# Kernel optimization log

Measured on AMD Instinct MI355X. Metric: run time of the kernel, lower is better.

## Reference

```python
import jax, jax.numpy as jnp
import numpy as np

N = 30000      # nodes
E = 480000     # edges (before self-loops)
G = 30         # graphs
DIN = 256      # input_dim
DH = 64        # hidden_dim (per-head out channels)
H = 8          # heads in layers 0,1; last layer has 1 head


def _glorot(key, shape):
    fan_in, fan_out = shape[0], shape[-1]
    s = jnp.sqrt(2.0 / (fan_in + fan_out))
    return jax.random.normal(key, shape, dtype=jnp.float32) * s


def setup_inputs() -> dict:
    key = jax.random.key(0)
    ks = jax.random.split(key, 32)
    inp = {
        'x': jax.random.normal(ks[0], (N, DIN), dtype=jnp.float32),
        'edge_index': jax.random.randint(ks[1], (2, E), 0, N, dtype=jnp.int64),
        'batch': jnp.sort(jax.random.randint(ks[2], (N,), 0, G, dtype=jnp.int64)),
        # GAT layer 0: in=256 -> 8 heads x 64
        'W0': _glorot(ks[3], (DIN, H * DH)),
        'as0': _glorot(ks[4], (H, DH)), 'ad0': _glorot(ks[5], (H, DH)),
        'b0': jnp.zeros((H * DH,), jnp.float32),
        # GAT layer 1: in=512 -> 8 heads x 64
        'W1': _glorot(ks[6], (H * DH, H * DH)),
        'as1': _glorot(ks[7], (H, DH)), 'ad1': _glorot(ks[8], (H, DH)),
        'b1': jnp.zeros((H * DH,), jnp.float32),
        # GAT layer 2: in=512 -> 1 head x 64
        'W2': _glorot(ks[9], (H * DH, DH)),
        'as2': _glorot(ks[10], (1, DH)), 'ad2': _glorot(ks[11], (1, DH)),
        'b2': jnp.zeros((DH,), jnp.float32),
        # batch norms (feature sizes match actual activations)
        'bn0_g': jnp.ones((H * DH,), jnp.float32), 'bn0_b': jnp.zeros((H * DH,), jnp.float32),
        'bn1_g': jnp.ones((H * DH,), jnp.float32), 'bn1_b': jnp.zeros((H * DH,), jnp.float32),
        'bn2_g': jnp.ones((DH,), jnp.float32), 'bn2_b': jnp.zeros((DH,), jnp.float32),
        'ln_g': jnp.ones((DH,), jnp.float32), 'ln_b': jnp.zeros((DH,), jnp.float32),
        'fc1_w': _glorot(ks[12], (DH, DH // 2)), 'fc1_b': jnp.zeros((DH // 2,), jnp.float32),
        'fc2_w': _glorot(ks[13], (DH // 2, 2)), 'fc2_b': jnp.zeros((2,), jnp.float32),
    }
    return inp


def _gat(x, src, dst, W, a_src, a_dst, bias, heads):
    # x: [N, Fin]; project to [N, heads, DH]
    h = (x @ W).reshape(N, heads, DH)
    s_src = jnp.sum(h * a_src, axis=-1)  # [N, heads]
    s_dst = jnp.sum(h * a_dst, axis=-1)  # [N, heads]
    e = jax.nn.leaky_relu(s_src[src] + s_dst[dst], 0.2)  # [Etot, heads]
    # segment softmax over edges grouped by destination node
    m = jax.ops.segment_max(e, dst, num_segments=N)
    p = jnp.exp(e - m[dst])
    denom = jax.ops.segment_sum(p, dst, num_segments=N)
    alpha = p / (denom[dst] + 1e-16)
    out = jax.ops.segment_sum(h[src] * alpha[:, :, None], dst, num_segments=N)
    return out.reshape(N, heads * DH) + bias


def _bn(x, g, b):
    m = jnp.mean(x, axis=0)
    v = jnp.var(x, axis=0)
    return (x - m) / jnp.sqrt(v + 1e-5) * g + b


def _forward(x, edge_index, batch,
             W0, as0, ad0, b0, W1, as1, ad1, b1, W2, as2, ad2, b2,
             bn0_g, bn0_b, bn1_g, bn1_b, bn2_g, bn2_b,
             ln_g, ln_b, fc1_w, fc1_b, fc2_w, fc2_b):
    loops = jnp.arange(N, dtype=edge_index.dtype)
    src = jnp.concatenate([edge_index[0], loops])
    dst = jnp.concatenate([edge_index[1], loops])
    # layer 0: 256 -> 512; no residual (dim mismatch)
    x1 = jax.nn.elu(_bn(_gat(x, src, dst, W0, as0, ad0, b0, H), bn0_g, bn0_b))
    # layer 1: 512 -> 512; residual
    x2 = jax.nn.elu(_bn(_gat(x1, src, dst, W1, as1, ad1, b1, H), bn1_g, bn1_b)) + x1
    # layer 2 (single head): 512 -> 64; no residual
    x3 = jax.nn.elu(_bn(_gat(x2, src, dst, W2, as2, ad2, b2, 1), bn2_g, bn2_b))
    # layer norm
    mu = jnp.mean(x3, axis=-1, keepdims=True)
    var = jnp.var(x3, axis=-1, keepdims=True)
    xl = (x3 - mu) / jnp.sqrt(var + 1e-5) * ln_g + ln_b
    # global mean pool over graphs
    sums = jax.ops.segment_sum(xl, batch, num_segments=G)
    cnt = jax.ops.segment_sum(jnp.ones((N, 1), xl.dtype), batch, num_segments=G)
    pooled = sums / jnp.maximum(cnt, 1.0)
    hdd = jax.nn.elu(pooled @ fc1_w + fc1_b)
    logits = hdd @ fc2_w + fc2_b
    return jax.nn.log_softmax(logits, axis=1)


def reference(x, edge_index, batch,
              W0, as0, ad0, b0, W1, as1, ad1, b1, W2, as2, ad2, b2,
              bn0_g, bn0_b, bn1_g, bn1_b, bn2_g, bn2_b,
              ln_g, ln_b, fc1_w, fc1_b, fc2_w, fc2_b):
    return _forward(x, edge_index, batch,
                    W0, as0, ad0, b0, W1, as1, ad1, b1, W2, as2, ad2, b2,
                    bn0_g, bn0_b, bn1_g, bn1_b, bn2_g, bn2_b,
                    ln_g, ln_b, fc1_w, fc1_b, fc2_w, fc2_b)
```

## Files before the change

### kernel.cpp

```cpp
#include <hip/hip_runtime.h>
#include <math.h>

#define NODES 30000
#define NEDGE 480000
#define ETOT  (NODES + NEDGE)
#define NGRAPH 30
#define DIN 256
#define DH 64
#define CAP 128

typedef __bf16 bf16x8 __attribute__((ext_vector_type(8)));
typedef float  f32x4  __attribute__((ext_vector_type(4)));

static __device__ __forceinline__ float elu_f(float x){ return x > 0.f ? x : expm1f(x); }
static __device__ __forceinline__ float bf_lo(unsigned v){ return __uint_as_float(v << 16); }
static __device__ __forceinline__ float bf_hi(unsigned v){ return __uint_as_float(v & 0xffff0000u); }
static __device__ __forceinline__ unsigned pack_bf2(float a, float b){
  __bf16 ob[2] = {(__bf16)a, (__bf16)b};
  return *(unsigned*)ob;
}
static __device__ __forceinline__ void load_lds16(const __bf16* g, __bf16* l){
  __builtin_amdgcn_global_load_lds(
      (const __attribute__((address_space(1))) void*)g,
      (__attribute__((address_space(3))) void*)l, 16, 0, 0);
}

__global__ void k_scan(const int* __restrict__ deg, int* __restrict__ rowptr){
  __shared__ int s[1024];
  int t = threadIdx.x;
  const int CH = (NODES + 1023) / 1024;
  int base = t * CH;
  int local = 0;
  for (int i = 0; i < CH; i++){ int idx = base + i; if (idx < NODES) local += deg[idx]; }
  s[t] = local; __syncthreads();
  for (int off = 1; off < 1024; off <<= 1){
    int v = (t >= off) ? s[t - off] : 0;
    __syncthreads();
    s[t] += v;
    __syncthreads();
  }
  int run = s[t] - local;
  for (int i = 0; i < CH; i++){
    int idx = base + i;
    if (idx < NODES){ rowptr[idx] = run; run += deg[idx]; }
  }
  if (t == 1023) rowptr[NODES] = s[1023];
}

__global__ void k_fill(const int* __restrict__ ei, const int* __restrict__ rowptr,
                       int* __restrict__ cursor, int* __restrict__ colA){
  int e = blockIdx.x*256 + threadIdx.x;
  if (e >= ETOT) return;
  int src, dst;
  if (e < NEDGE){ src = ei[e]; dst = ei[NEDGE + e]; }
  else          { src = e - NEDGE; dst = src; }
  int pos = atomicAdd(&cursor[dst], 1);
  colA[rowptr[dst] + pos] = src;
}

#define NCAST4 (NODES*DIN/4)
#define TW0 (512*256)
#define TW1 (512*512)
#define TW2 (64*512)
#define PREPW (NCAST4 + TW0 + TW1 + TW2)
__global__ void k_prep(const float* __restrict__ x, __bf16* __restrict__ xb0,
                       const float* __restrict__ W0, const float* __restrict__ W1,
                       const float* __restrict__ W2, __bf16* __restrict__ Wt0,
                       __bf16* __restrict__ Wt1, __bf16* __restrict__ Wt2,
                       const int* __restrict__ ei, int* __restrict__ deg){
  int idx = blockIdx.x*256 + threadIdx.x;
  if (idx < NCAST4){
    float4 v = ((const float4*)x)[idx];
    __bf16 o[4] = {(__bf16)v.x, (__bf16)v.y, (__bf16)v.z, (__bf16)v.w};
    *(uint2*)(xb0 + (size_t)idx*4) = *(const uint2*)o;
    return;
  }
  int j = idx - NCAST4;
  if (j < TW0){
    int n = j >> 8, k = j & 255;
    Wt0[j] = (__bf16)W0[(size_t)k*512 + n];
    return;
  }
  j -= TW0;
  if (j < TW1){
    int n = j >> 9, k = j & 511;
    Wt1[j] = (__bf16)W1[(size_t)k*512 + n];
    return;
  }
  j -= TW1;
  if (j < TW2){
    int n = j >> 9, k = j & 511;
    Wt2[j] = (__bf16)W2[(size_t)k*64 + n];
    return;
  }
  j -= TW2;
  if (j < ETOT){
    int dst = (j < NEDGE) ? ei[NEDGE + j] : (j - NEDGE);
    atomicAdd(&deg[dst], 1);
  }
}

__global__ __launch_bounds__(256) void k_gemm_bf16(const __bf16* __restrict__ A,
    const __bf16* __restrict__ Bt, __bf16* __restrict__ C,
    const float* __restrict__ asrc, const float* __restrict__ adst,
    float* __restrict__ ssrc, float* __restrict__ sdst, int heads,
    int M, int N, int K){
  __shared__ __align__(16) __bf16 As[128*64];
  __shared__ __align__(16) __bf16 Bs[128*64];
  int tid  = threadIdx.x;
  int lane = tid & 63, wave = tid >> 6;
  int wr = wave >> 1, wc = wave & 1;
  int q = lane >> 4, r = lane & 15;
  int rowBase = blockIdx.y * 128, colBase = blockIdx.x * 128;
  f32x4 acc[4][4] = {};
  for (int k0 = 0; k0 < K; k0 += 64){
    #pragma unroll
    for (int p = 0; p < 4; p++){
      int lin = p*256 + tid;
      int rr = lin >> 3, ko = (lin & 7) * 8;
      int gr = rowBase + rr; if (gr >= M) gr = M - 1;
      load_lds16(A + (size_t)gr*K + k0 + ko, As + lin*8);
      int gn = colBase + rr; if (gn >= N) gn = N - 1;
      load_lds16(Bt + (size_t)gn*K + k0 + ko, Bs + lin*8);
    }
    __syncthreads();
    #pragma unroll
    for (int kk = 0; kk < 2; kk++){
      bf16x8 af[4], bfr[4];
      #pragma unroll
      for (int i = 0; i < 4; i++) af[i]  = *(const bf16x8*)(&As[(wr*64 + i*16 + r)*64 + kk*32 + q*8]);
      #pragma unroll
      for (int j = 0; j < 4; j++) bfr[j] = *(const bf16x8*)(&Bs[(wc*64 + j*16 + r)*64 + kk*32 + q*8]);
      #pragma unroll
      for (int i = 0; i < 4; i++)
        #pragma unroll
        for (int j = 0; j < 4; j++)
          acc[i][j] = __builtin_amdgcn_mfma_f32_16x16x32_bf16(af[i], bfr[j], acc[i][j], 0, 0, 0);
    }
    __syncthreads();
  }
  #pragma unroll
  for (int i = 0; i < 4; i++){
    #pragma unroll
    for (int j = 0; j < 4; j++){
      int col = colBase + wc*64 + j*16 + r;
      if (col >= N) continue;
      #pragma unroll
      for (int v = 0; v < 4; v++){
        int row = rowBase + wr*64 + i*16 + q*4 + v;
        if (row < M) C[(size_t)row*N + col] = (__bf16)acc[i][j][v];
      }
    }
  }
  int colW = colBase + wc*64;
  if (colW < N){
    int hb = colW >> 6;
    float a_s[4], a_d[4];
    #pragma unroll
    for (int j = 0; j < 4; j++){
      a_s[j] = asrc[hb*64 + j*16 + r];
      a_d[j] = adst[hb*64 + j*16 + r];
    }
    #pragma unroll
    for (int i = 0; i < 4; i++){
      #pragma unroll
      for (int v = 0; v < 4; v++){
        float s1 = 0.f, s2 = 0.f;
        #pragma unroll
        for (int j = 0; j < 4; j++){
          float av = acc[i][j][v];
          s1 += av * a_s[j];
          s2 += av * a_d[j];
        }
        #pragma unroll
        for (int off = 1; off < 16; off <<= 1){
          s1 += __shfl_xor(s1, off, 64);
          s2 += __shfl_xor(s2, off, 64);
        }
        if (r == 0){
          int row = rowBase + wr*64 + i*16 + q*4 + v;
          if (row < M){
            ssrc[(size_t)row*heads + hb] = s1;
            sdst[(size_t)row*heads + hb] = s2;
          }
        }
      }
    }
  }
}

__global__ __launch_bounds__(256) void k_gatagg8(const __bf16* __restrict__ hb,
    const float* __restrict__ ssrc, const float* __restrict__ sdst,
    const int* __restrict__ rowptr, const int* __restrict__ colA,
    const float* __restrict__ bias, __bf16* __restrict__ outb){
  int n = blockIdx.x;
  int t = threadIdx.x;
  __shared__ int ecol[CAP];
  __shared__ float p[CAP][9];
  __shared__ float racc[3][8][64];
  __shared__ float dhv[8], sdsh[8], mh[8];
  int base = rowptr[n];
  int deg = rowptr[n+1] - base;
  if (t < 8) sdsh[t] = sdst[(size_t)n*8 + t];
  __syncthreads();
  int g = t >> 5, l32 = t & 31;
  int quar = t >> 6, l = t & 63;
  int f8 = l * 8;
  int hh = l >> 3;
  if (deg <= CAP){
    if (t < deg){
      int c = colA[base + t];
      ecol[t] = c;
      const float4* sp = (const float4*)(ssrc + (size_t)c*8);
      float4 s0 = sp[0], s1 = sp[1];
      float v;
      v = s0.x + sdsh[0]; p[t][0] = v > 0.f ? v : 0.2f*v;
      v = s0.y + sdsh[1]; p[t][1] = v > 0.f ? v : 0.2f*v;
      v = s0.z + sdsh[2]; p[t][2] = v > 0.f ? v : 0.2f*v;
      v = s0.w + sdsh[3]; p[t][3] = v > 0.f ? v : 0.2f*v;
      v = s1.x + sdsh[4]; p[t][4] = v > 0.f ? v : 0.2f*v;
      v = s1.y + sdsh[5]; p[t][5] = v > 0.f ? v : 0.2f*v;
      v = s1.z + sdsh[6]; p[t][6] = v > 0.f ? v : 0.2f*v;
      v = s1.w + sdsh[7]; p[t][7] = v > 0.f ? v : 0.2f*v;
    }
    __syncthreads();
    {
      float m = -1e30f;
      for (int e = l32; e < deg; e += 32) m = fmaxf(m, p[e][g]);
      #pragma unroll
      for (int off = 1; off < 32; off <<= 1) m = fmaxf(m, __shfl_xor(m, off, 64));
      float d = 0.f;
      for (int e = l32; e < deg; e += 32){ float xv = __expf(p[e][g] - m); p[e][g] = xv; d += xv; }
      #pragma unroll
      for (int off = 1; off < 32; off <<= 1) d += __shfl_xor(d, off, 64);
      if (l32 == 0) dhv[g] = 1.f / (d + 1e-16f);
    }
    __syncthreads();
    float a0[8] = {}, a1[8] = {};
    int e = quar;
    for (; e + 12 < deg; e += 16){
      int c0 = ecol[e], c1 = ecol[e+4], c2 = ecol[e+8], c3 = ecol[e+12];
      float p0 = p[e][hh], p1 = p[e+4][hh], p2 = p[e+8][hh], p3 = p[e+12][hh];
      uint4 v0 = *(const uint4*)(hb + (size_t)c0*512 + f8);
      uint4 v1 = *(const uint4*)(hb + (size_t)c1*512 + f8);
      uint4 v2 = *(const uint4*)(hb + (size_t)c2*512 + f8);
      uint4 v3 = *(const uint4*)(hb + (size_t)c3*512 + f8);
      unsigned w0[4] = {v0.x, v0.y, v0.z, v0.w};
      unsigned w1[4] = {v1.x, v1.y, v1.z, v1.w};
      unsigned w2[4] = {v2.x, v2.y, v2.z, v2.w};
      unsigned w3[4] = {v3.x, v3.y, v3.z, v3.w};
      #pragma unroll
      for (int j = 0; j < 4; j++){
        a0[2*j]   += p0*bf_lo(w0[j]); a0[2*j+1] += p0*bf_hi(w0[j]);
        a1[2*j]   += p1*bf_lo(w1[j]); a1[2*j+1] += p1*bf_hi(w1[j]);
        a0[2*j]   += p2*bf_lo(w2[j]); a0[2*j+1] += p2*bf_hi(w2[j]);
        a1[2*j]   += p3*bf_lo(w3[j]); a1[2*j+1] += p3*bf_hi(w3[j]);
      }
    }
    for (; e + 4 < deg; e += 8){
      float pe0 = p[e][hh], pe1 = p[e+4][hh];
      uint4 v0 = *(const uint4*)(hb + (size_t)ecol[e]*512 + f8);
      uint4 v1 = *(const uint4*)(hb + (size_t)ecol[e+4]*512 + f8);
      unsigned w0[4] = {v0.x, v0.y, v0.z, v0.w};
      unsigned w1[4] = {v1.x, v1.y, v1.z, v1.w};
      #pragma unroll
      for (int j = 0; j < 4; j++){
        a0[2*j]   += pe0*bf_lo(w0[j]); a0[2*j+1] += pe0*bf_hi(w0[j]);
        a1[2*j]   += pe1*bf_lo(w1[j]); a1[2*j+1] += pe1*bf_hi(w1[j]);
      }
    }
    for (; e < deg; e += 4){
      float pe = p[e][hh];
      uint4 v = *(const uint4*)(hb + (size_t)ecol[e]*512 + f8);
      unsigned w[4] = {v.x, v.y, v.z, v.w};
      #pragma unroll
      for (int j = 0; j < 4; j++){
        a0[2*j] += pe*bf_lo(w[j]); a0[2*j+1] += pe*bf_hi(w[j]);
      }
    }
    #pragma unroll
    for (int j = 0; j < 8; j++) a0[j] += a1[j];
    if (quar){
      #pragma unroll
      for (int j = 0; j < 8; j++) racc[quar-1][j][l] = a0[j];
    }
    __syncthreads();
    if (quar == 0){
      float rcp = dhv[hh];
      float4 bb0 = *(const float4*)(bias + f8);
      float4 bb1 = *(const float4*)(bias + f8 + 4);
      float bb[8] = {bb0.x, bb0.y, bb0.z, bb0.w, bb1.x, bb1.y, bb1.z, bb1.w};
      __bf16 ob[8];
      #pragma unroll
      for (int j = 0; j < 8; j++){
        float s = a0[j] + racc[0][j][l] + racc[1][j][l] + racc[2][j][l];
        ob[j] = (__bf16)(s*rcp + bb[j]);
      }
      *(uint4*)(outb + (size_t)n*512 + f8) = *(const uint4*)ob;
    }
  } else {
    float m = -1e30f;
    for (int e = l32; e < deg; e += 32){
      int c = colA[base + e];
      float sc = ssrc[(size_t)c*8 + g] + sdsh[g];
      sc = sc > 0.f ? sc : 0.2f*sc;
      m = fmaxf(m, sc);
    }
    #pragma unroll
    for (int off = 1; off < 32; off <<= 1) m = fmaxf(m, __shfl_xor(m, off, 64));
    if (l32 == 0) mh[g] = m;
    __syncthreads();
    float d = 0.f;
    float mm = mh[g];
    for (int e = l32; e < deg; e += 32){
      int c = colA[base + e];
      float sc = ssrc[(size_t)c*8 + g] + sdsh[g];
      sc = sc > 0.f ? sc : 0.2f*sc;
      d += __expf(sc - mm);
    }
    #pragma unroll
    for (int off = 1; off < 32; off <<= 1) d += __shfl_xor(d, off, 64);
    if (l32 == 0) dhv[g] = 1.f / (d + 1e-16f);
    __syncthreads();
    float a0[8] = {};
    float mhh = mh[hh];
    float sdd = sdsh[hh];
    for (int e = quar; e < deg; e += 4){
      int c = colA[base + e];
      float sc = ssrc[(size_t)c*8 + hh] + sdd;
      sc = sc > 0.f ? sc : 0.2f*sc;
      float pe = __expf(sc - mhh);
      uint4 v = *(const uint4*)(hb + (size_t)c*512 + f8);
      unsigned w[4] = {v.x, v.y, v.z, v.w};
      #pragma unroll
      for (int j = 0; j < 4; j++){
        a0[2*j] += pe*bf_lo(w[j]); a0[2*j+1] += pe*bf_hi(w[j]);
      }
    }
    if (quar){
      #pragma unroll
      for (int j = 0; j < 8; j++) racc[quar-1][j][l] = a0[j];
    }
    __syncthreads();
    if (quar == 0){
      float rcp = dhv[hh];
      float4 bb0 = *(const float4*)(bias + f8);
      float4 bb1 = *(const float4*)(bias + f8 + 4);
      float bb[8] = {bb0.x, bb0.y, bb0.z, bb0.w, bb1.x, bb1.y, bb1.z, bb1.w};
      __bf16 ob[8];
      #pragma unroll
      for (int j = 0; j < 8; j++){
        float s = a0[j] + racc[0][j][l] + racc[1][j][l] + racc[2][j][l];
        ob[j] = (__bf16)(s*rcp + bb[j]);
      }
      *(uint4*)(outb + (size_t)n*512 + f8) = *(const uint4*)ob;
    }
  }
}

__global__ __launch_bounds__(256) void k_gatagg1(const __bf16* __restrict__ hb,
    const float* __restrict__ ssrc, const float* __restrict__ sdst,
    const int* __restrict__ rowptr, const int* __restrict__ colA,
    const float* __restrict__ bias, __bf16* __restrict__ outb){
  int n = blockIdx.x;
  int t = threadIdx.x;
  __shared__ int ecol[CAP];
  __shared__ float p[CAP];
  __shared__ float racc[8][64];
  __shared__ float dhv1, mh1, sds;
  int base = rowptr[n];
  int deg = rowptr[n+1] - base;
  if (t == 0) sds = sdst[n];
  __syncthreads();
  int g = t >> 5, l = t & 31;
  if (deg <= CAP){
    if (t < deg){
      int c = colA[base + t];
      ecol[t] = c;
      float sc = ssrc[c] + sds;
      p[t] = sc > 0.f ? sc : 0.2f*sc;
    }
    __syncthreads();
    if (t < 64){
      float m = -1e30f;
      for (int e = t; e < deg; e += 64) m = fmaxf(m, p[e]);
      #pragma unroll
      for (int off = 1; off < 64; off <<= 1) m = fmaxf(m, __shfl_xor(m, off, 64));
      float d = 0.f;
      for (int e = t; e < deg; e += 64){ float xv = __expf(p[e] - m); p[e] = xv; d += xv; }
      #pragma unroll
      for (int off = 1; off < 64; off <<= 1) d += __shfl_xor(d, off, 64);
      if (t == 0) dhv1 = 1.f / (d + 1e-16f);
    }
    __syncthreads();
    float a0 = 0.f, a1 = 0.f, b0v = 0.f, b1v = 0.f;
    int e = g;
    for (; e + 8 < deg; e += 16){
      int c0 = ecol[e], c1 = ecol[e+8];
      float pe0 = p[e], pe1 = p[e+8];
      unsigned v0 = *(const unsigned*)(hb + (size_t)c0*64 + l*2);
      unsigned v1 = *(const unsigned*)(hb + (size_t)c1*64 + l*2);
      a0  += pe0*bf_lo(v0); a1  += pe0*bf_hi(v0);
      b0v += pe1*bf_lo(v1); b1v += pe1*bf_hi(v1);
    }
    for (; e < deg; e += 8){
      float pe = p[e];
      unsigned v = *(const unsigned*)(hb + (size_t)ecol[e]*64 + l*2);
      a0 += pe*bf_lo(v); a1 += pe*bf_hi(v);
    }
    a0 += b0v; a1 += b1v;
    racc[g][l*2] = a0; racc[g][l*2+1] = a1;
    __syncthreads();
    if (t < 32){
      float s0 = 0.f, s1 = 0.f;
      #pragma unroll
      for (int g2 = 0; g2 < 8; g2++){ s0 += racc[g2][t*2]; s1 += racc[g2][t*2+1]; }
      float rcp = dhv1;
      float o0 = s0*rcp + bias[t*2], o1 = s1*rcp + bias[t*2+1];
      *(unsigned*)(outb + (size_t)n*64 + t*2) = pack_bf2(o0, o1);
    }
  } else {
    if (t < 64){
      float m = -1e30f;
      for (int e = t; e < deg; e += 64){
        int c = colA[base + e];
        float sc = ssrc[c] + sds;
        sc = sc > 0.f ? sc : 0.2f*sc;
        m = fmaxf(m, sc);
      }
      #pragma unroll
      for (int off = 1; off < 64; off <<= 1) m = fmaxf(m, __shfl_xor(m, off, 64));
      if (t == 0) mh1 = m;
    }
    __syncthreads();
    if (t < 64){
      float d = 0.f;
      for (int e = t; e < deg; e += 64){
        int c = colA[base + e];
        float sc = ssrc[c] + sds;
        sc = sc > 0.f ? sc : 0.2f*sc;
        d += __expf(sc - mh1);
      }
      #pragma unroll
      for (int off = 1; off < 64; off <<= 1) d += __shfl_xor(d, off, 64);
      if (t == 0) dhv1 = 1.f / (d + 1e-16f);
    }
    __syncthreads();
    float a0 = 0.f, a1 = 0.f;
    float mm = mh1;
    for (int e = g; e < deg; e += 8){
      int c = colA[base + e];
      float sc = ssrc[c] + sds;
      sc = sc > 0.f ? sc : 0.2f*sc;
      float pe = __expf(sc - mm);
      unsigned v = *(const unsigned*)(hb + (size_t)c*64 + l*2);
      a0 += pe*bf_lo(v); a1 += pe*bf_hi(v);
    }
    racc[g][l*2] = a0; racc[g][l*2+1] = a1;
    __syncthreads();
    if (t < 32){
      float s0 = 0.f, s1 = 0.f;
      #pragma unroll
      for (int g2 = 0; g2 < 8; g2++){ s0 += racc[g2][t*2]; s1 += racc[g2][t*2+1]; }
      float rcp = dhv1;
      float o0 = s0*rcp + bias[t*2], o1 = s1*rcp + bias[t*2+1];
      *(unsigned*)(outb + (size_t)n*64 + t*2) = pack_bf2(o0, o1);
    }
  }
}

__global__ __launch_bounds__(256) void k_bnstat1(const __bf16* __restrict__ xb,
    float* __restrict__ partial, int F){
  int t = threadIdx.x;
  int OCT = F >> 3;
  int RPB = 256 / OCT;
  int o = t & (OCT - 1), r = t / OCT;
  int NB = gridDim.x;
  float s[8] = {}, q[8] = {};
  int step = NB * RPB;
  for (int n = blockIdx.x*RPB + r; n < NODES; n += step){
    uint4 v = *(const uint4*)(xb + (size_t)n*F + o*8);
    unsigned vv[4] = {v.x, v.y, v.z, v.w};
    #pragma unroll
    for (int j = 0; j < 4; j++){
      float lo = bf_lo(vv[j]), hi = bf_hi(vv[j]);
      s[2*j]   += lo; q[2*j]   += lo*lo;
      s[2*j+1] += hi; q[2*j+1] += hi*hi;
    }
  }
  __shared__ float red[256][17];
  #pragma unroll
  for (int j = 0; j < 8; j++){ red[t][j] = s[j]; red[t][8+j] = q[j]; }
  __syncthreads();
  for (int st = RPB >> 1; st > 0; st >>= 1){
    if (r < st){
      #pragma unroll
      for (int j = 0; j < 16; j++) red[t][j] += red[t + st*OCT][j];
    }
    __syncthreads();
  }
  if (r == 0){
    #pragma unroll
    for (int j = 0; j < 8; j++){
      partial[(size_t)(o*8 + j)*NB + blockIdx.x]     = red[t][j];
      partial[(size_t)(F + o*8 + j)*NB + blockIdx.x] = red[t][8 + j];
    }
  }
}

__global__ void k_bnstat2(const float* __restrict__ partial, float* __restrict__ sum,
                          float* __restrict__ sumsq, int F, int NB){
  int row = blockIdx.x;
  int t = threadIdx.x;
  float a = 0.f;
  for (int i = t; i < NB; i += 64) a += partial[(size_t)row*NB + i];
  #pragma unroll
  for (int off = 1; off < 64; off <<= 1) a += __shfl_xor(a, off, 64);
  if (t == 0){
    if (row < F) sum[row] = a;
    else         sumsq[row - F] = a;
  }
}

__global__ __launch_bounds__(256) void k_bnapply_b(const __bf16* __restrict__ xb,
    const float* __restrict__ sum, const float* __restrict__ sumsq,
    const float* __restrict__ g, const float* __restrict__ b,
    const __bf16* __restrict__ res, __bf16* __restrict__ y, int rows){
  int t = threadIdx.x;
  int o8 = (t & 63) * 8;
  int rw = t >> 6;
  float sm[8], sq[8], gg[8], bb[8];
  *(float4*)sm     = *(const float4*)(sum + o8);
  *(float4*)(sm+4) = *(const float4*)(sum + o8 + 4);
  *(float4*)sq     = *(const float4*)(sumsq + o8);
  *(float4*)(sq+4) = *(const float4*)(sumsq + o8 + 4);
  *(float4*)gg     = *(const float4*)(g + o8);
  *(float4*)(gg+4) = *(const float4*)(g + o8 + 4);
  *(float4*)bb     = *(const float4*)(b + o8);
  *(float4*)(bb+4) = *(const float4*)(b + o8 + 4);
  const float inv_n = 1.f / (float)NODES;
  float sc[8], sh[8];
  #pragma unroll
  for (int j = 0; j < 8; j++){
    float m = sm[j]*inv_n;
    float v = sq[j]*inv_n - m*m;
    sc[j] = gg[j]*rsqrtf(v + 1e-5f);
    sh[j] = bb[j] - m*sc[j];
  }
  int nend = min(blockIdx.x*rows + rows, NODES);
  for (int n = blockIdx.x*rows + rw; n < nend; n += 4){
    size_t off = (size_t)n*512 + o8;
    uint4 v = *(const uint4*)(xb + off);
    unsigned w[4] = {v.x, v.y, v.z, v.w};
    float ov[8];
    #pragma unroll
    for (int j = 0; j < 4; j++){
      ov[2*j]   = elu_f(bf_lo(w[j])*sc[2*j]   + sh[2*j]);
      ov[2*j+1] = elu_f(bf_hi(w[j])*sc[2*j+1] + sh[2*j+1]);
    }
    if (res){
      uint4 rv = *(const uint4*)(res + off);
      unsigned rw4[4] = {rv.x, rv.y, rv.z, rv.w};
      #pragma unroll
      for (int j = 0; j < 4; j++){
        ov[2*j] += bf_lo(rw4[j]); ov[2*j+1] += bf_hi(rw4[j]);
      }
    }
    __bf16 ob[8];
    #pragma unroll
    for (int j = 0; j < 8; j++) ob[j] = (__bf16)ov[j];
    *(uint4*)(y + off) = *(const uint4*)ob;
  }
}

__global__ void k_bn_elu_ln_b(const __bf16* __restrict__ xb, const float* __restrict__ sum,
    const float* __restrict__ sumsq, const float* __restrict__ g, const float* __restrict__ b,
    const float* __restrict__ lg, const float* __restrict__ lb, float* __restrict__ y){
  int t = threadIdx.x;
  int l = t & 31, sub = t >> 5;
  int n = blockIdx.x*8 + sub;
  float2 sm = *(const float2*)(sum + l*2);
  float2 sq = *(const float2*)(sumsq + l*2);
  float2 gg = *(const float2*)(g + l*2);
  float2 bb = *(const float2*)(b + l*2);
  const float inv_n = 1.f / (float)NODES;
  float m0 = sm.x*inv_n, m1 = sm.y*inv_n;
  float va0 = sq.x*inv_n - m0*m0, va1 = sq.y*inv_n - m1*m1;
  float sc0 = gg.x * rsqrtf(va0 + 1e-5f), sc1 = gg.y * rsqrtf(va1 + 1e-5f);
  float sh0 = bb.x - m0*sc0, sh1 = bb.y - m1*sc1;
  unsigned v = *(const unsigned*)(xb + (size_t)n*64 + l*2);
  float x0 = elu_f(bf_lo(v)*sc0 + sh0);
  float x1 = elu_f(bf_hi(v)*sc1 + sh1);
  float s = x0 + x1;
  #pragma unroll
  for (int off = 1; off < 32; off <<= 1) s += __shfl_xor(s, off, 64);
  float mean = s * (1.f/64.f);
  float d0 = x0 - mean, d1 = x1 - mean;
  float qq = d0*d0 + d1*d1;
  #pragma unroll
  for (int off = 1; off < 32; off <<= 1) qq += __shfl_xor(qq, off, 64);
  float var = qq * (1.f/64.f);
  float inv = rsqrtf(var + 1e-5f);
  float2 o = make_float2(d0*inv*lg[l*2] + lb[l*2], d1*inv*lg[l*2+1] + lb[l*2+1]);
  *(float2*)(y + (size_t)n*64 + l*2) = o;
}

static __device__ int lbound(const int* a, int n, int v){
  int lo = 0, hi = n;
  while (lo < hi){ int mid = (lo + hi) >> 1; if (a[mid] < v) lo = mid + 1; else hi = mid; }
  return lo;
}

__global__ void k_pool(const float* __restrict__ xl, const int* __restrict__ batch,
                       float* __restrict__ pooled){
  int g = blockIdx.x;
  int t = threadIdx.x;
  int lo = lbound(batch, NODES, g);
  int hi = lbound(batch, NODES, g+1);
  int f = t & 63, grp = t >> 6;
  float acc = 0.f;
  for (int n = lo + grp; n < hi; n += 4) acc += xl[(size_t)n*DH + f];
  __shared__ float red[4][64];
  red[grp][f] = acc;
  __syncthreads();
  if (grp == 0){
    float s = red[0][f] + red[1][f] + red[2][f] + red[3][f];
    int cnt = hi - lo;
    pooled[g*DH + f] = s / fmaxf((float)cnt, 1.f);
  }
}

__global__ void k_head(const float* __restrict__ pooled, const float* __restrict__ w1,
                       const float* __restrict__ b1, const float* __restrict__ w2,
                       const float* __restrict__ b2, float* __restrict__ out){
  int g = threadIdx.x;
  if (g >= NGRAPH) return;
  const float* pd = pooled + g*DH;
  float hdd[32];
  for (int j = 0; j < 32; j++){
    float s = b1[j];
    for (int d = 0; d < DH; d++) s += pd[d]*w1[d*32 + j];
    hdd[j] = elu_f(s);
  }
  float l0 = b2[0], l1 = b2[1];
  for (int j = 0; j < 32; j++){ l0 += hdd[j]*w2[j*2]; l1 += hdd[j]*w2[j*2 + 1]; }
  float m = fmaxf(l0, l1);
  float lse = m + logf(expf(l0 - m) + expf(l1 - m));
  out[g*2]     = l0 - lse;
  out[g*2 + 1] = l1 - lse;
}

extern "C" void kernel_launch(void* const* d_in, const int* in_sizes, int n_in,
                              void* d_out, int out_size, void* d_ws, size_t ws_size,
                              hipStream_t stream){
  const float* x    = (const float*)d_in[0];
  const int*   ei   = (const int*)d_in[1];
  const int*   batch= (const int*)d_in[2];
  const float* W0   = (const float*)d_in[3];
  const float* as0  = (const float*)d_in[4];
  const float* ad0  = (const float*)d_in[5];
  const float* b0   = (const float*)d_in[6];
  const float* W1   = (const float*)d_in[7];
  const float* as1  = (const float*)d_in[8];
  const float* ad1  = (const float*)d_in[9];
  const float* b1   = (const float*)d_in[10];
  const float* W2   = (const float*)d_in[11];
  const float* as2  = (const float*)d_in[12];
  const float* ad2  = (const float*)d_in[13];
  const float* b2   = (const float*)d_in[14];
  const float* bn0g = (const float*)d_in[15];
  const float* bn0b = (const float*)d_in[16];
  const float* bn1g = (const float*)d_in[17];
  const float* bn1b = (const float*)d_in[18];
  const float* bn2g = (const float*)d_in[19];
  const float* bn2b = (const float*)d_in[20];
  const float* lng  = (const float*)d_in[21];
  const float* lnb  = (const float*)d_in[22];
  const float* fc1w = (const float*)d_in[23];
  const float* fc1b = (const float*)d_in[24];
  const float* fc2w = (const float*)d_in[25];
  const float* fc2b = (const float*)d_in[26];
  float* out = (float*)d_out;

  char* w = (char*)d_ws;
  auto alloc = [&](size_t bytes) -> char* {
    char* p = w; w += (bytes + 255) & ~(size_t)255; return p;
  };
  __bf16* xb0   = (__bf16*)alloc((size_t)NODES*DIN*2);
  __bf16* hbuf  = (__bf16*)alloc((size_t)NODES*512*2);
  __bf16* gbuf  = (__bf16*)alloc((size_t)NODES*512*2);
  __bf16* x1b   = (__bf16*)alloc((size_t)NODES*512*2);
  __bf16* x2b   = (__bf16*)alloc((size_t)NODES*512*2);
  __bf16* Wt0   = (__bf16*)alloc((size_t)TW0*2);
  __bf16* Wt1   = (__bf16*)alloc((size_t)TW1*2);
  __bf16* Wt2   = (__bf16*)alloc((size_t)TW2*2);
  float*  ssrc  = (float*)alloc((size_t)NODES*8*4);
  float*  sdst  = (float*)alloc((size_t)NODES*8*4);
  float*  xl    = (float*)alloc((size_t)NODES*DH*4);
  float*  pooled= (float*)alloc(NGRAPH*DH*4);
  int*    rowptr= (int*)alloc((NODES+1)*4);
  int*    colA  = (int*)alloc((size_t)ETOT*4);
  float*  partial=(float*)alloc((size_t)2*512*512*4);
  float*  sum0  = (float*)alloc(512*4);
  float*  sq0   = (float*)alloc(512*4);
  float*  sum1  = (float*)alloc(512*4);
  float*  sq1   = (float*)alloc(512*4);
  float*  sum2  = (float*)alloc(64*4);
  float*  sq2   = (float*)alloc(64*4);
  char* zbase  = w;
  int*   deg   = (int*)alloc(NODES*4);
  int*   cursor= (int*)alloc(NODES*4);
  size_t zbytes = (size_t)(w - zbase);
  hipMemsetAsync(zbase, 0, zbytes, stream);

  const int prep_total = PREPW + ETOT;
  k_prep<<<(prep_total + 255)/256, 256, 0, stream>>>(x, xb0, W0, W1, W2, Wt0, Wt1, Wt2, ei, deg);
  k_scan<<<1, 1024, 0, stream>>>(deg, rowptr);
  const int eb = (ETOT + 255)/256;
  k_fill<<<eb, 256, 0, stream>>>(ei, rowptr, cursor, colA);

  const int mb128 = (NODES + 127)/128;
  const int nb8 = (NODES + 7)/8;
  const int nb16 = (NODES + 15)/16;

  k_gemm_bf16<<<dim3(4, mb128), 256, 0, stream>>>(xb0, Wt0, hbuf, as0, ad0, ssrc, sdst, 8, NODES, 512, DIN);
  k_gatagg8<<<NODES, 256, 0, stream>>>(hbuf, ssrc, sdst, rowptr, colA, b0, gbuf);
  k_bnstat1<<<512, 256, 0, stream>>>(gbuf, partial, 512);
  k_bnstat2<<<1024, 64, 0, stream>>>(partial, sum0, sq0, 512, 512);
  k_bnapply_b<<<nb16, 256, 0, stream>>>(gbuf, sum0, sq0, bn0g, bn0b, nullptr, x1b, 16);

  k_gemm_bf16<<<dim3(4, mb128), 256, 0, stream>>>(x1b, Wt1, hbuf, as1, ad1, ssrc, sdst, 8, NODES, 512, 512);
  k_gatagg8<<<NODES, 256, 0, stream>>>(hbuf, ssrc, sdst, rowptr, colA, b1, gbuf);
  k_bnstat1<<<512, 256, 0, stream>>>(gbuf, partial, 512);
  k_bnstat2<<<1024, 64, 0, stream>>>(partial, sum1, sq1, 512, 512);
  k_bnapply_b<<<nb16, 256, 0, stream>>>(gbuf, sum1, sq1, bn1g, bn1b, x1b, x2b, 16);

  k_gemm_bf16<<<dim3(1, mb128), 256, 0, stream>>>(x2b, Wt2, hbuf, as2, ad2, ssrc, sdst, 1, NODES, 64, 512);
  k_gatagg1<<<NODES, 256, 0, stream>>>(hbuf, ssrc, sdst, rowptr, colA, b2, gbuf);
  k_bnstat1<<<256, 256, 0, stream>>>(gbuf, partial, 64);
  k_bnstat2<<<128, 64, 0, stream>>>(partial, sum2, sq2, 64, 256);
  k_bn_elu_ln_b<<<nb8, 256, 0, stream>>>(gbuf, sum2, sq2, bn2g, bn2b, lng, lnb, xl);

  k_pool<<<NGRAPH, 256, 0, stream>>>(xl, batch, pooled);
  k_head<<<1, 32, 0, stream>>>(pooled, fc1w, fc1b, fc2w, fc2b, out);
}
```

Measured before the change: 694.4 us.

## Widen GAT aggregation blocks to 8 waves and fuse mean-pool into LN kernel

The 8-head aggregation kernel now runs 512 threads (8 wavefronts) per node instead of 256. Each wave computes the softmax for one head and takes an 8-way share of the edge gather, with cross-wave reduction through a larger LDS buffer. Separately, the final BN/ELU/LayerNorm kernel now accumulates per-graph sums with atomics, removing the xl intermediate and the separate pool kernel; the head kernel applies the count division. This trades fewer in-flight loads per thread and more atomics for more wavefronts per node and one less launch and round trip.

```diff
diff --git a/kernel.cpp b/kernel.cpp
--- a/kernel.cpp
+++ b/kernel.cpp
@@ -189,7 +189,7 @@
   }
 }
 
-__global__ __launch_bounds__(256) void k_gatagg8(const __bf16* __restrict__ hb,
+__global__ __launch_bounds__(512) void k_gatagg8(const __bf16* __restrict__ hb,
     const float* __restrict__ ssrc, const float* __restrict__ sdst,
     const int* __restrict__ rowptr, const int* __restrict__ colA,
     const float* __restrict__ bias, __bf16* __restrict__ outb){
@@ -197,14 +197,13 @@
   int t = threadIdx.x;
   __shared__ int ecol[CAP];
   __shared__ float p[CAP][9];
-  __shared__ float racc[3][8][64];
+  __shared__ float racc[7][8][64];
   __shared__ float dhv[8], sdsh[8], mh[8];
   int base = rowptr[n];
   int deg = rowptr[n+1] - base;
   if (t < 8) sdsh[t] = sdst[(size_t)n*8 + t];
   __syncthreads();
-  int g = t >> 5, l32 = t & 31;
-  int quar = t >> 6, l = t & 63;
+  int w = t >> 6, l = t & 63;
   int f8 = l * 8;
   int hh = l >> 3;
   if (deg <= CAP){
@@ -226,66 +225,48 @@
     __syncthreads();
     {
       float m = -1e30f;
-      for (int e = l32; e < deg; e += 32) m = fmaxf(m, p[e][g]);
-      #pragma unroll
-      for (int off = 1; off < 32; off <<= 1) m = fmaxf(m, __shfl_xor(m, off, 64));
+      for (int e = l; e < deg; e += 64) m = fmaxf(m, p[e][w]);
+      #pragma unroll
+      for (int off = 1; off < 64; off <<= 1) m = fmaxf(m, __shfl_xor(m, off, 64));
       float d = 0.f;
-      for (int e = l32; e < deg; e += 32){ float xv = __expf(p[e][g] - m); p[e][g] = xv; d += xv; }
-      #pragma unroll
-      for (int off = 1; off < 32; off <<= 1) d += __shfl_xor(d, off, 64);
-      if (l32 == 0) dhv[g] = 1.f / (d + 1e-16f);
+      for (int e = l; e < deg; e += 64){ float xv = __expf(p[e][w] - m); p[e][w] = xv; d += xv; }
+      #pragma unroll
+      for (int off = 1; off < 64; off <<= 1) d += __shfl_xor(d, off, 64);
+      if (l == 0) dhv[w] = 1.f / (d + 1e-16f);
     }
     __syncthreads();
     float a0[8] = {}, a1[8] = {};
-    int e = quar;
-    for (; e + 12 < deg; e += 16){
-      int c0 = ecol[e], c1 = ecol[e+4], c2 = ecol[e+8], c3 = ecol[e+12];
-      float p0 = p[e][hh], p1 = p[e+4][hh], p2 = p[e+8][hh], p3 = p[e+12][hh];
+    int e = w;
+    for (; e + 8 < deg; e += 16){
+      int c0 = ecol[e], c1 = ecol[e+8];
+      float p0 = p[e][hh], p1 = p[e+8][hh];
       uint4 v0 = *(const uint4*)(hb + (size_t)c0*512 + f8);
       uint4 v1 = *(const uint4*)(hb + (size_t)c1*512 + f8);
-      uint4 v2 = *(const uint4*)(hb + (size_t)c2*512 + f8);
-      uint4 v3 = *(const uint4*)(hb + (size_t)c3*512 + f8);
       unsigned w0[4] = {v0.x, v0.y, v0.z, v0.w};
       unsigned w1[4] = {v1.x, v1.y, v1.z, v1.w};
-      unsigned w2[4] = {v2.x, v2.y, v2.z, v2.w};
-      unsigned w3[4] = {v3.x, v3.y, v3.z, v3.w};
       #pragma unroll
       for (int j = 0; j < 4; j++){
         a0[2*j]   += p0*bf_lo(w0[j]); a0[2*j+1] += p0*bf_hi(w0[j]);
         a1[2*j]   += p1*bf_lo(w1[j]); a1[2*j+1] += p1*bf_hi(w1[j]);
-        a0[2*j]   += p2*bf_lo(w2[j]); a0[2*j+1] += p2*bf_hi(w2[j]);
-        a1[2*j]   += p3*bf_lo(w3[j]); a1[2*j+1] += p3*bf_hi(w3[j]);
-      }
-    }
-    for (; e + 4 < deg; e += 8){
-      float pe0 = p[e][hh], pe1 = p[e+4][hh];
-      uint4 v0 = *(const uint4*)(hb + (size_t)ecol[e]*512 + f8);
-      uint4 v1 = *(const uint4*)(hb + (size_t)ecol[e+4]*512 + f8);
-      unsigned w0[4] = {v0.x, v0.y, v0.z, v0.w};
-      unsigned w1[4] = {v1.x, v1.y, v1.z, v1.w};
-      #pragma unroll
-      for (int j = 0; j < 4; j++){
-        a0[2*j]   += pe0*bf_lo(w0[j]); a0[2*j+1] += pe0*bf_hi(w0[j]);
-        a1[2*j]   += pe1*bf_lo(w1[j]); a1[2*j+1] += pe1*bf_hi(w1[j]);
-      }
-    }
-    for (; e < deg; e += 4){
+      }
+    }
+    for (; e < deg; e += 8){
       float pe = p[e][hh];
       uint4 v = *(const uint4*)(hb + (size_t)ecol[e]*512 + f8);
-      unsigned w[4] = {v.x, v.y, v.z, v.w};
+      unsigned ww[4] = {v.x, v.y, v.z, v.w};
       #pragma unroll
       for (int j = 0; j < 4; j++){
-        a0[2*j] += pe*bf_lo(w[j]); a0[2*j+1] += pe*bf_hi(w[j]);
+        a0[2*j] += pe*bf_lo(ww[j]); a0[2*j+1] += pe*bf_hi(ww[j]);
       }
     }
     #pragma unroll
     for (int j = 0; j < 8; j++) a0[j] += a1[j];
-    if (quar){
-      #pragma unroll
-      for (int j = 0; j < 8; j++) racc[quar-1][j][l] = a0[j];
-    }
-    __syncthreads();
-    if (quar == 0){
+    if (w){
+      #pragma unroll
+      for (int j = 0; j < 8; j++) racc[w-1][j][l] = a0[j];
+    }
+    __syncthreads();
+    if (w == 0){
       float rcp = dhv[hh];
       float4 bb0 = *(const float4*)(bias + f8);
       float4 bb1 = *(const float4*)(bias + f8 + 4);
@@ -293,56 +274,58 @@
       __bf16 ob[8];
       #pragma unroll
       for (int j = 0; j < 8; j++){
-        float s = a0[j] + racc[0][j][l] + racc[1][j][l] + racc[2][j][l];
+        float s = a0[j];
+        #pragma unroll
+        for (int k = 0; k < 7; k++) s += racc[k][j][l];
         ob[j] = (__bf16)(s*rcp + bb[j]);
       }
       *(uint4*)(outb + (size_t)n*512 + f8) = *(const uint4*)ob;
     }
   } else {
     float m = -1e30f;
-    for (int e = l32; e < deg; e += 32){
+    for (int e = l; e < deg; e += 64){
       int c = colA[base + e];
-      float sc = ssrc[(size_t)c*8 + g] + sdsh[g];
+      float sc = ssrc[(size_t)c*8 + w] + sdsh[w];
       sc = sc > 0.f ? sc : 0.2f*sc;
       m = fmaxf(m, sc);
     }
     #pragma unroll
-    for (int off = 1; off < 32; off <<= 1) m = fmaxf(m, __shfl_xor(m, off, 64));
-    if (l32 == 0) mh[g] = m;
+    for (int off = 1; off < 64; off <<= 1) m = fmaxf(m, __shfl_xor(m, off, 64));
+    if (l == 0) mh[w] = m;
     __syncthreads();
     float d = 0.f;
-    float mm = mh[g];
-    for (int e = l32; e < deg; e += 32){
+    float mm = mh[w];
+    for (int e = l; e < deg; e += 64){
       int c = colA[base + e];
-      float sc = ssrc[(size_t)c*8 + g] + sdsh[g];
+      float sc = ssrc[(size_t)c*8 + w] + sdsh[w];
       sc = sc > 0.f ? sc : 0.2f*sc;
       d += __expf(sc - mm);
     }
     #pragma unroll
-    for (int off = 1; off < 32; off <<= 1) d += __shfl_xor(d, off, 64);
-    if (l32 == 0) dhv[g] = 1.f / (d + 1e-16f);
+    for (int off = 1; off < 64; off <<= 1) d += __shfl_xor(d, off, 64);
+    if (l == 0) dhv[w] = 1.f / (d + 1e-16f);
     __syncthreads();
     float a0[8] = {};
     float mhh = mh[hh];
     float sdd = sdsh[hh];
-    for (int e = quar; e < deg; e += 4){
+    for (int e = w; e < deg; e += 8){
       int c = colA[base + e];
       float sc = ssrc[(size_t)c*8 + hh] + sdd;
       sc = sc > 0.f ? sc : 0.2f*sc;
       float pe = __expf(sc - mhh);
       uint4 v = *(const uint4*)(hb + (size_t)c*512 + f8);
-      unsigned w[4] = {v.x, v.y, v.z, v.w};
+      unsigned ww[4] = {v.x, v.y, v.z, v.w};
       #pragma unroll
       for (int j = 0; j < 4; j++){
-        a0[2*j] += pe*bf_lo(w[j]); a0[2*j+1] += pe*bf_hi(w[j]);
-      }
-    }
-    if (quar){
-      #pragma unroll
-      for (int j = 0; j < 8; j++) racc[quar-1][j][l] = a0[j];
-    }
-    __syncthreads();
-    if (quar == 0){
+        a0[2*j] += pe*bf_lo(ww[j]); a0[2*j+1] += pe*bf_hi(ww[j]);
+      }
+    }
+    if (w){
+      #pragma unroll
+      for (int j = 0; j < 8; j++) racc[w-1][j][l] = a0[j];
+    }
+    __syncthreads();
+    if (w == 0){
       float rcp = dhv[hh];
       float4 bb0 = *(const float4*)(bias + f8);
       float4 bb1 = *(const float4*)(bias + f8 + 4);
@@ -350,7 +333,9 @@
       __bf16 ob[8];
       #pragma unroll
       for (int j = 0; j < 8; j++){
-        float s = a0[j] + racc[0][j][l] + racc[1][j][l] + racc[2][j][l];
+        float s = a0[j];
+        #pragma unroll
+        for (int k = 0; k < 7; k++) s += racc[k][j][l];
         ob[j] = (__bf16)(s*rcp + bb[j]);
       }
       *(uint4*)(outb + (size_t)n*512 + f8) = *(const uint4*)ob;
@@ -573,9 +558,10 @@
   }
 }
 
-__global__ void k_bn_elu_ln_b(const __bf16* __restrict__ xb, const float* __restrict__ sum,
+__global__ void k_bn_elu_ln_pool(const __bf16* __restrict__ xb, const float* __restrict__ sum,
     const float* __restrict__ sumsq, const float* __restrict__ g, const float* __restrict__ b,
-    const float* __restrict__ lg, const float* __restrict__ lb, float* __restrict__ y){
+    const float* __restrict__ lg, const float* __restrict__ lb,
+    const int* __restrict__ batch, float* __restrict__ pooled){
   int t = threadIdx.x;
   int l = t & 31, sub = t >> 5;
   int n = blockIdx.x*8 + sub;
@@ -601,8 +587,25 @@
   for (int off = 1; off < 32; off <<= 1) qq += __shfl_xor(qq, off, 64);
   float var = qq * (1.f/64.f);
   float inv = rsqrtf(var + 1e-5f);
-  float2 o = make_float2(d0*inv*lg[l*2] + lb[l*2], d1*inv*lg[l*2+1] + lb[l*2+1]);
-  *(float2*)(y + (size_t)n*64 + l*2) = o;
+  float o0 = d0*inv*lg[l*2] + lb[l*2];
+  float o1 = d1*inv*lg[l*2+1] + lb[l*2+1];
+  __shared__ float sv[8][64];
+  __shared__ int gid[8];
+  sv[sub][l*2] = o0; sv[sub][l*2+1] = o1;
+  if (l == 0) gid[sub] = batch[n];
+  __syncthreads();
+  if (t < 64){
+    int g0 = gid[0];
+    if (gid[7] == g0){
+      float acc = 0.f;
+      #pragma unroll
+      for (int r = 0; r < 8; r++) acc += sv[r][t];
+      atomicAdd(&pooled[g0*64 + t], acc);
+    } else {
+      #pragma unroll
+      for (int r = 0; r < 8; r++) atomicAdd(&pooled[gid[r]*64 + t], sv[r][t]);
+    }
+  }
 }
 
 static __device__ int lbound(const int* a, int n, int v){
@@ -611,31 +614,17 @@
   return lo;
 }
 
-__global__ void k_pool(const float* __restrict__ xl, const int* __restrict__ batch,
-                       float* __restrict__ pooled){
-  int g = blockIdx.x;
-  int t = threadIdx.x;
+__global__ void k_head(const float* __restrict__ pooled, const int* __restrict__ batch,
+                       const float* __restrict__ w1, const float* __restrict__ b1,
+                       const float* __restrict__ w2, const float* __restrict__ b2,
+                       float* __restrict__ out){
+  int g = threadIdx.x;
+  if (g >= NGRAPH) return;
   int lo = lbound(batch, NODES, g);
   int hi = lbound(batch, NODES, g+1);
-  int f = t & 63, grp = t >> 6;
-  float acc = 0.f;
-  for (int n = lo + grp; n < hi; n += 4) acc += xl[(size_t)n*DH + f];
-  __shared__ float red[4][64];
-  red[grp][f] = acc;
-  __syncthreads();
-  if (grp == 0){
-    float s = red[0][f] + red[1][f] + red[2][f] + red[3][f];
-    int cnt = hi - lo;
-    pooled[g*DH + f] = s / fmaxf((float)cnt, 1.f);
-  }
-}
-
-__global__ void k_head(const float* __restrict__ pooled, const float* __restrict__ w1,
-                       const float* __restrict__ b1, const float* __restrict__ w2,
-                       const float* __restrict__ b2, float* __restrict__ out){
-  int g = threadIdx.x;
-  if (g >= NGRAPH) return;
-  const float* pd = pooled + g*DH;
+  float inv_cnt = 1.f / fmaxf((float)(hi - lo), 1.f);
+  float pd[64];
+  for (int d = 0; d < 64; d++) pd[d] = pooled[g*DH + d] * inv_cnt;
   float hdd[32];
   for (int j = 0; j < 32; j++){
     float s = b1[j];
@@ -696,8 +685,6 @@
   __bf16* Wt2   = (__bf16*)alloc((size_t)TW2*2);
   float*  ssrc  = (float*)alloc((size_t)NODES*8*4);
   float*  sdst  = (float*)alloc((size_t)NODES*8*4);
-  float*  xl    = (float*)alloc((size_t)NODES*DH*4);
-  float*  pooled= (float*)alloc(NGRAPH*DH*4);
   int*    rowptr= (int*)alloc((NODES+1)*4);
   int*    colA  = (int*)alloc((size_t)ETOT*4);
   float*  partial=(float*)alloc((size_t)2*512*512*4);
@@ -710,6 +697,7 @@
   char* zbase  = w;
   int*   deg   = (int*)alloc(NODES*4);
   int*   cursor= (int*)alloc(NODES*4);
+  float* pooled= (float*)alloc(NGRAPH*DH*4);
   size_t zbytes = (size_t)(w - zbase);
   hipMemsetAsync(zbase, 0, zbytes, stream);
 
@@ -724,13 +712,13 @@
   const int nb16 = (NODES + 15)/16;
 
   k_gemm_bf16<<<dim3(4, mb128), 256, 0, stream>>>(xb0, Wt0, hbuf, as0, ad0, ssrc, sdst, 8, NODES, 512, DIN);
-  k_gatagg8<<<NODES, 256, 0, stream>>>(hbuf, ssrc, sdst, rowptr, colA, b0, gbuf);
+  k_gatagg8<<<NODES, 512, 0, stream>>>(hbuf, ssrc, sdst, rowptr, colA, b0, gbuf);
   k_bnstat1<<<512, 256, 0, stream>>>(gbuf, partial, 512);
   k_bnstat2<<<1024, 64, 0, stream>>>(partial, sum0, sq0, 512, 512);
   k_bnapply_b<<<nb16, 256, 0, stream>>>(gbuf, sum0, sq0, bn0g, bn0b, nullptr, x1b, 16);
 
   k_gemm_bf16<<<dim3(4, mb128), 256, 0, stream>>>(x1b, Wt1, hbuf, as1, ad1, ssrc, sdst, 8, NODES, 512, 512);
-  k_gatagg8<<<NODES, 256, 0, stream>>>(hbuf, ssrc, sdst, rowptr, colA, b1, gbuf);
+  k_gatagg8<<<NODES, 512, 0, stream>>>(hbuf, ssrc, sdst, rowptr, colA, b1, gbuf);
   k_bnstat1<<<512, 256, 0, stream>>>(gbuf, partial, 512);
   k_bnstat2<<<1024, 64, 0, stream>>>(partial, sum1, sq1, 512, 512);
   k_bnapply_b<<<nb16, 256, 0, stream>>>(gbuf, sum1, sq1, bn1g, bn1b, x1b, x2b, 16);
@@ -739,8 +727,7 @@
   k_gatagg1<<<NODES, 256, 0, stream>>>(hbuf, ssrc, sdst, rowptr, colA, b2, gbuf);
   k_bnstat1<<<256, 256, 0, stream>>>(gbuf, partial, 64);
   k_bnstat2<<<128, 64, 0, stream>>>(partial, sum2, sq2, 64, 256);
-  k_bn_elu_ln_b<<<nb8, 256, 0, stream>>>(gbuf, sum2, sq2, bn2g, bn2b, lng, lnb, xl);
-
-  k_pool<<<NGRAPH, 256, 0, stream>>>(xl, batch, pooled);
-  k_head<<<1, 32, 0, stream>>>(pooled, fc1w, fc1b, fc2w, fc2b, out);
-}
+  k_bn_elu_ln_pool<<<nb8, 256, 0, stream>>>(gbuf, sum2, sq2, bn2g, bn2b, lng, lnb, batch, pooled);
+
+  k_head<<<1, 32, 0, stream>>>(pooled, batch, fc1w, fc1b, fc2w, fc2b, out);
+}
```

After: 772.9 us. 11.3% more time.
